# Optimization experiments

Hardware: AMD Instinct MI355X
Metric: run time of the kernel (lower is better)

The kernel has to match this reference:

```python
import jax, jax.numpy as jnp
import numpy as np

N_VOX = 200_000
C = 64
B, G = 2, 128  # batch size, grid resolution per axis
K = 27         # 3x3x3 kernel volume
EPS = 1e-5


def _build_coords_and_kernel_map(seed=0):
    """Build unique voxel coords on a [B,G,G,G] grid and the 27-offset kernel map.

    nbr[i, k] = row index of the voxel at coord[i] + offset[k], or N_VOX if absent
    (sentinel row that gathers zeros). This mirrors MinkowskiEngine's
    coordinate-hash in/out kernel maps for a stride-1 conv.
    """
    rng = np.random.default_rng(seed)
    total = B * G * G * G
    keys = np.sort(rng.choice(total, size=N_VOX, replace=False).astype(np.int64))
    z = keys % G
    y = (keys // G) % G
    x = (keys // (G * G)) % G
    b = keys // (G * G * G)
    offs = [(dx, dy, dz) for dx in (-1, 0, 1) for dy in (-1, 0, 1) for dz in (-1, 0, 1)]
    nbr = np.full((N_VOX, K), N_VOX, dtype=np.int64)
    for k, (dx, dy, dz) in enumerate(offs):
        nx, ny, nz = x + dx, y + dy, z + dz
        valid = (nx >= 0) & (nx < G) & (ny >= 0) & (ny < G) & (nz >= 0) & (nz < G)
        nkey = ((b * G + nx) * G + ny) * G + nz
        pos = np.clip(np.searchsorted(keys, nkey), 0, N_VOX - 1)
        found = valid & (keys[pos] == nkey)
        nbr[:, k] = np.where(found, pos, N_VOX)
    return jnp.asarray(nbr)


def setup_inputs() -> dict:
    key = jax.random.key(0)
    ks = jax.random.split(key, 12)
    w_scale = 1.0 / np.sqrt(K * C)
    inp = {
        "feats": jax.random.normal(ks[0], (N_VOX, C), jnp.float32),
        "nbr": _build_coords_and_kernel_map(),
        "W1": jax.random.normal(ks[1], (K, C, C), jnp.float32) * w_scale,
        "g1": 1.0 + 0.1 * jax.random.normal(ks[2], (C,), jnp.float32),
        "b1": 0.1 * jax.random.normal(ks[3], (C,), jnp.float32),
        "m1": 0.1 * jax.random.normal(ks[4], (C,), jnp.float32),
        "v1": jax.random.uniform(ks[5], (C,), jnp.float32, 0.5, 1.5),
        "W2": jax.random.normal(ks[6], (K, C, C), jnp.float32) * w_scale,
        "g2": 1.0 + 0.1 * jax.random.normal(ks[7], (C,), jnp.float32),
        "b2": 0.1 * jax.random.normal(ks[8], (C,), jnp.float32),
        "m2": 0.1 * jax.random.normal(ks[9], (C,), jnp.float32),
        "v2": jax.random.uniform(ks[10], (C,), jnp.float32, 0.5, 1.5),
    }
    return inp


def _bn(x, g, b, m, v):
    # MinkowskiBatchNorm, eval mode: per-channel affine with running stats
    return (x - m) * (g * jax.lax.rsqrt(v + EPS)) + b


def _sparse_conv(feats, nbr, W):
    # gather-GEMM-scatter sparse 3D conv over the precomputed kernel map.
    # Sentinel index N_VOX gathers the appended zero row (missing neighbor).
    fpad = jnp.concatenate([feats, jnp.zeros((1, feats.shape[1]), feats.dtype)], axis=0)
    out = jnp.zeros((feats.shape[0], W.shape[2]), feats.dtype)
    for k in range(W.shape[0]):  # fixed 27-tap loop (structural, not data dim)
        out = out + fpad[nbr[:, k]] @ W[k]
    return out


def reference(feats, nbr, W1, g1, b1, m1, v1, W2, g2, b2, m2, v2):
    h = jax.nn.relu(_bn(_sparse_conv(feats, nbr, W1), g1, b1, m1, v1))
    h = _bn(_sparse_conv(h, nbr, W2), g2, b2, m2, v2)
    # in_channels == out_channels and stride == 1 -> identity shortcut
    return jax.nn.relu(h + feats)
```

## Files before the change

### kernel.cpp

```cpp
#include <hip/hip_runtime.h>
#include <hip/hip_bf16.h>

#define NVOX 200000
#define NTAP 27
#define OSTR 68
#define ROWB 128
#define VPB  128

typedef __bf16          bf16x8 __attribute__((ext_vector_type(8)));
typedef unsigned short  u16x8  __attribute__((ext_vector_type(8)));
typedef float           f32x4  __attribute__((ext_vector_type(4)));

#define FB_BYTES    ((size_t)(NVOX + 1) * ROWB)
#define WSHUF_BYTES (NTAP * 2 * 4 * 64 * 16)
#define FB_OFF      0
#define H_OFF       (FB_BYTES)
#define WS1_OFF     (2 * FB_BYTES)
#define WS2_OFF     (WS1_OFF + WSHUF_BYTES)
#define FLAG_OFF    (WS2_OFF + WSHUF_BYTES)

static __device__ __forceinline__ unsigned short f2bf_bits(float f) {
    __hip_bfloat16 h = __float2bfloat16(f);
    union { __hip_bfloat16 h; unsigned short u; } u; u.h = h; return u.u;
}
static __device__ __forceinline__ float bf2f(unsigned short s) {
    union { float f; unsigned u; } u; u.u = ((unsigned)s) << 16; return u.f;
}
static __device__ __forceinline__ float ld_param(const void* p, int c, int isbf) {
    return isbf ? bf2f(((const unsigned short*)p)[c]) : ((const float*)p)[c];
}
static __device__ __forceinline__ void gload_lds16(const void* gp, void* lp) {
    __builtin_amdgcn_global_load_lds(
        (const __attribute__((address_space(1))) void*)gp,
        (__attribute__((address_space(3))) void*)lp, 16, 0, 0);
}
static __device__ __forceinline__ int wave_isbf(const unsigned* v1w) {
    int l = threadIdx.x & 63;
    int ok = 1;
    if (l < 32) {
        unsigned w = v1w[l], lo = w & 0xFFFFu, hi = w >> 16;
        ok = (lo >= 0x3F00u && lo <= 0x3FC0u && hi >= 0x3F00u && hi <= 0x3FC0u);
    }
    return __all(ok);
}

__global__ __launch_bounds__(256)
void prep_kernel(const void* __restrict__ feats,
                 const void* __restrict__ W1, const void* __restrict__ W2,
                 const unsigned* __restrict__ v1w, const unsigned* __restrict__ nbrw,
                 uint4* __restrict__ fbuf, uint4* __restrict__ hbuf,
                 uint4* __restrict__ Ws1, uint4* __restrict__ Ws2,
                 int* __restrict__ flags) {
    const int bx = blockIdx.x;
    if (bx < 6250) {
        const int isbf = wave_isbf(v1w);
        size_t t = (size_t)bx * 256 + threadIdx.x;
        if (isbf) {
            fbuf[t] = ((const uint4*)feats)[t];
        } else {
            float4 a = ((const float4*)feats)[2 * t];
            float4 b = ((const float4*)feats)[2 * t + 1];
            union { uint4 q; unsigned short u[8]; } o;
            o.u[0] = f2bf_bits(a.x); o.u[1] = f2bf_bits(a.y);
            o.u[2] = f2bf_bits(a.z); o.u[3] = f2bf_bits(a.w);
            o.u[4] = f2bf_bits(b.x); o.u[5] = f2bf_bits(b.y);
            o.u[6] = f2bf_bits(b.z); o.u[7] = f2bf_bits(b.w);
            fbuf[t] = o.q;
        }
    } else if (bx < 6358) {
        const int isbf = wave_isbf(v1w);
        int t = (bx - 6250) * 256 + threadIdx.x;
        const void* W = (t < 13824) ? W1 : W2;
        uint4* Ws     = (t < 13824) ? Ws1 : Ws2;
        int f = (t < 13824) ? t : t - 13824;
        int k  = f / 512;
        int r  = f % 512;
        int kc = r / 256;
        int r2 = r % 256;
        int nc = r2 / 64;
        int l  = r2 % 64;
        int quad = l >> 4, li = l & 15;
        unsigned short tmp[8];
#pragma unroll
        for (int j = 0; j < 8; ++j) {
            int off = k * 4096 + (kc * 32 + quad * 8 + j) * 64 + (nc * 16 + li);
            tmp[j] = isbf ? ((const unsigned short*)W)[off]
                          : f2bf_bits(((const float*)W)[off]);
        }
        uint4 v;
        v.x = (unsigned)tmp[0] | ((unsigned)tmp[1] << 16);
        v.y = (unsigned)tmp[2] | ((unsigned)tmp[3] << 16);
        v.z = (unsigned)tmp[4] | ((unsigned)tmp[5] << 16);
        v.w = (unsigned)tmp[6] | ((unsigned)tmp[7] << 16);
        Ws[f] = v;
    } else {
        int t = threadIdx.x;
        if (t < 64) {
            int isbf = wave_isbf(v1w);
            int n64ok = 1;
#pragma unroll
            for (int i = 0; i < 8; ++i)
                if (nbrw[2 * (t * 8 + i) + 1] != 0u) n64ok = 0;
            int n64 = __all(n64ok);
            if (t == 0) { flags[0] = isbf; flags[1] = n64; }
        }
        uint4 z = make_uint4(0u, 0u, 0u, 0u);
        if (t >= 64 && t < 72) fbuf[(size_t)NVOX * 8 + (t - 64)] = z;
        if (t >= 72 && t < 80) hbuf[(size_t)NVOX * 8 + (t - 72)] = z;
    }
}

#define STG(kk, bp) do {                                                    \
    if ((mga >> (kk)) & 1) {                                                \
        int ia_ = bad0 ? NVOX : nbrG[o0 + (kk) * tmul];                     \
        int ib_ = bad1 ? NVOX : nbrG[o1 + (kk) * tmul];                     \
        gload_lds16(srcB + (size_t)ia_ * ROWB + f0 * 16,                    \
                    (void*)((bp) + w * 256));                               \
        gload_lds16(srcB + (size_t)ib_ * ROWB + f1 * 16,                    \
                    (void*)((bp) + w * 256 + 64));                          \
    }                                                                       \
    if ((mgb >> (kk)) & 1) {                                                \
        int ic_ = bad2 ? NVOX : nbrG[o2 + (kk) * tmul];                     \
        int id_ = bad3 ? NVOX : nbrG[o3 + (kk) * tmul];                     \
        gload_lds16(srcB + (size_t)ic_ * ROWB + f2 * 16,                    \
                    (void*)((bp) + w * 256 + 128));                         \
        gload_lds16(srcB + (size_t)id_ * ROWB + f3 * 16,                    \
                    (void*)((bp) + w * 256 + 192));                         \
    } } while (0)

#define LOADB(kk, B0r, B1r) do {                                            \
    B0r = Ws[(kk) * 512 + w * 64 + l];                                      \
    B1r = Ws[(kk) * 512 + 256 + w * 64 + l];                                \
} while (0)

#define COMPUTE(kk, bp, B0, B1) do {                                        \
    _Pragma("unroll")                                                       \
    for (int g = 0; g < 8; ++g) {                                           \
        if ((mg[g] >> (kk)) & 1) {                                          \
            bf16x8 a0_ = *(const bf16x8*)((bp) + ro0[g]);                   \
            bf16x8 a1_ = *(const bf16x8*)((bp) + ro1[g]);                   \
            acc[g] = __builtin_amdgcn_mfma_f32_16x16x32_bf16(a0_, B0, acc[g], 0, 0, 0); \
            acc[g] = __builtin_amdgcn_mfma_f32_16x16x32_bf16(a1_, B1, acc[g], 0, 0, 0); \
        }                                                                   \
    }                                                                       \
} while (0)

__global__ __launch_bounds__(256, 4)
void conv_bn_kernel(const uint4* __restrict__ srcV,
                    const void* __restrict__ nbr,
                    const bf16x8* __restrict__ Ws,
                    const void* __restrict__ gg, const void* __restrict__ bb,
                    const void* __restrict__ mm, const void* __restrict__ vv,
                    const u16x8* __restrict__ resid,
                    const int* __restrict__ flags,
                    void* __restrict__ dst, int final_out) {
    __shared__ __align__(16) int smi[VPB * OSTR];
    int*   maskLDS = smi;
    uint4* at0     = (uint4*)(smi + 8);
    uint4* at1     = at0 + 1024;
    float* outLDS  = (float*)smi;

    const int tid  = threadIdx.x;
    const int nwg  = gridDim.x;
    const int orig = blockIdx.x;
    const int qq   = nwg >> 3, rr = nwg & 7;
    const int xcd  = orig & 7, idx = orig >> 3;
    const int bid  = (xcd < rr ? xcd * (qq + 1) : rr * (qq + 1) + (xcd - rr) * qq) + idx;
    const int base = bid * VPB;

    const int isbf = flags[0];
    const int n64  = flags[1];
    const char* srcB = (const char*)srcV;

    const int* nbrG = (const int*)nbr;
    const int  tmul = n64 ? 2 : 1;
    const int  smul = NTAP * tmul;

    if (tid < 8) maskLDS[tid] = 0;
    __syncthreads();

    if (tid < NTAP * 8) {
        int k = tid >> 3, g = tid & 7;
        int mn = 0x7fffffff;
#pragma unroll
        for (int r = 0; r < 16; ++r) {
            int vx = base + g * 16 + r;
            int safe = vx < NVOX ? vx : NVOX - 1;
            int v = nbrG[safe * smul + k * tmul];
            if (vx >= NVOX) v = NVOX;
            mn = min(mn, v);
        }
        if (mn < NVOX) atomicOr(&maskLDS[g], 1 << k);
    }
    __syncthreads();

    const int w = tid >> 6, l = tid & 63;
    const int quad = l >> 4, li = l & 15;

    int mg[8];
#pragma unroll
    for (int g = 0; g < 8; ++g) mg[g] = __builtin_amdgcn_readfirstlane(maskLDS[g]);
    const int mga = __builtin_amdgcn_readfirstlane(maskLDS[2 * w]);
    const int mgb = __builtin_amdgcn_readfirstlane(maskLDS[2 * w + 1]);

    int o_[4], f_[4], bad_[4];
#pragma unroll
    for (int j = 0; j < 4; ++j) {
        int s  = w * 256 + j * 64 + l;
        int r  = s >> 3;
        f_[j]  = (s - r) & 7;
        int vx = base + r;
        bad_[j] = vx >= NVOX;
        o_[j]  = (bad_[j] ? NVOX - 1 : vx) * smul;
    }
    const int o0 = o_[0], o1 = o_[1], o2 = o_[2], o3 = o_[3];
    const int f0 = f_[0], f1 = f_[1], f2 = f_[2], f3 = f_[3];
    const int bad0 = bad_[0], bad1 = bad_[1], bad2 = bad_[2], bad3 = bad_[3];

    int ro0[8], ro1[8];
#pragma unroll
    for (int g = 0; g < 8; ++g) {
        int row = g * 16 + li;
        ro0[g] = row * 8 + ((quad + row) & 7);
        ro1[g] = row * 8 + ((quad + 4 + row) & 7);
    }

    f32x4 acc[8];
#pragma unroll
    for (int g = 0; g < 8; ++g) acc[g] = (f32x4){0.f, 0.f, 0.f, 0.f};

    bf16x8 xB0, xB1, yB0, yB1;

    STG(0, at0);
    LOADB(0, xB0, xB1);
    __syncthreads();

    for (int k = 0; k < 26; k += 2) {
        STG(k + 1, at1);
        LOADB(k + 1, yB0, yB1);
        COMPUTE(k, at0, xB0, xB1);
        __syncthreads();
        STG(k + 2, at0);
        LOADB(k + 2, xB0, xB1);
        COMPUTE(k + 1, at1, yB0, yB1);
        __syncthreads();
    }
    COMPUTE(26, at0, xB0, xB1);

    const int c = w * 16 + li;
    float scale = ld_param(gg, c, isbf) * rsqrtf(ld_param(vv, c, isbf) + 1e-5f);
    float offs  = ld_param(bb, c, isbf) - ld_param(mm, c, isbf) * scale;

    __syncthreads();
#pragma unroll
    for (int g = 0; g < 8; ++g)
#pragma unroll
        for (int r = 0; r < 4; ++r)
            outLDS[(g * 16 + quad * 4 + r) * OSTR + c] = acc[g][r] * scale + offs;
    __syncthreads();

#pragma unroll
    for (int half = 0; half < 2; ++half) {
        int trow = half * 64 + (tid >> 2), cc = tid & 3;
        long grow = base + trow;
        if (grow < NVOX) {
            const float4* lp = (const float4*)&outLDS[trow * OSTR + cc * 16];
            float4 q0 = lp[0], q1 = lp[1], q2 = lp[2], q3 = lp[3];
            float vals[16] = {q0.x, q0.y, q0.z, q0.w, q1.x, q1.y, q1.z, q1.w,
                              q2.x, q2.y, q2.z, q2.w, q3.x, q3.y, q3.z, q3.w};

            if (resid) {
                const u16x8* rp = resid + grow * 8 + cc * 2;
                u16x8 r0v = rp[0], r1v = rp[1];
#pragma unroll
                for (int j = 0; j < 8; ++j) { vals[j] += bf2f(r0v[j]); vals[8 + j] += bf2f(r1v[j]); }
            }
#pragma unroll
            for (int j = 0; j < 16; ++j) vals[j] = fmaxf(vals[j], 0.f);

            const int store_bf = (!final_out) || isbf;
            if (store_bf) {
                u16x8 o0v, o1v;
#pragma unroll
                for (int j = 0; j < 8; ++j) { o0v[j] = f2bf_bits(vals[j]); o1v[j] = f2bf_bits(vals[8 + j]); }
                u16x8* dp = (u16x8*)dst + grow * 8 + cc * 2;
                dp[0] = o0v; dp[1] = o1v;
            } else {
                float4* dp = (float4*)dst + grow * 16 + cc * 4;
                dp[0] = (float4){vals[0], vals[1], vals[2], vals[3]};
                dp[1] = (float4){vals[4], vals[5], vals[6], vals[7]};
                dp[2] = (float4){vals[8], vals[9], vals[10], vals[11]};
                dp[3] = (float4){vals[12], vals[13], vals[14], vals[15]};
            }
        }
    }
}

extern "C" void kernel_launch(void* const* d_in, const int* in_sizes, int n_in,
                              void* d_out, int out_size, void* d_ws, size_t ws_size,
                              hipStream_t stream) {
    const void* feats = d_in[0];
    const void* nbr   = d_in[1];
    const void* W1    = d_in[2];
    const void* g1    = d_in[3];
    const void* b1    = d_in[4];
    const void* m1    = d_in[5];
    const void* v1    = d_in[6];
    const void* W2    = d_in[7];
    const void* g2    = d_in[8];
    const void* b2    = d_in[9];
    const void* m2    = d_in[10];
    const void* v2    = d_in[11];

    char* ws = (char*)d_ws;
    uint4* fbuf = (uint4*)(ws + FB_OFF);
    uint4* hbuf = (uint4*)(ws + H_OFF);
    uint4* Ws1  = (uint4*)(ws + WS1_OFF);
    uint4* Ws2  = (uint4*)(ws + WS2_OFF);
    int*   flags = (int*)(ws + FLAG_OFF);

    prep_kernel<<<dim3(6359), dim3(256), 0, stream>>>(
        feats, W1, W2, (const unsigned*)v1, (const unsigned*)nbr,
        fbuf, hbuf, Ws1, Ws2, flags);

    const int nblk = (NVOX + VPB - 1) / VPB;
    conv_bn_kernel<<<dim3(nblk), dim3(256), 0, stream>>>(
        fbuf, nbr, (const bf16x8*)Ws1, g1, b1, m1, v1,
        nullptr, flags, hbuf, 0);

    conv_bn_kernel<<<dim3(nblk), dim3(256), 0, stream>>>(
        hbuf, nbr, (const bf16x8*)Ws2, g2, b2, m2, v2,
        (const u16x8*)fbuf, flags, d_out, 1);
}
```

Before: 285.3 us.

## Halve LDS staging buffers by pipelining half-tiles to raise occupancy

The gather staging is split into two 64-row halves. One half is loaded into one LDS buffer while the other half is computed, and the same per-tap weight registers serve both halves. This halves shared memory per block (128x68 to 64x68 ints) and raises launch bounds from 4 to 6 blocks per CU, to hide gather latency through occupancy. The cost is twice as many barriers per tap, less prefetch distance, and an epilogue done in two passes.

```diff
diff --git a/kernel.cpp b/kernel.cpp
--- a/kernel.cpp
+++ b/kernel.cpp
@@ -110,22 +110,14 @@
     }
 }
 
-#define STG(kk, bp) do {                                                    \
-    if ((mga >> (kk)) & 1) {                                                \
-        int ia_ = bad0 ? NVOX : nbrG[o0 + (kk) * tmul];                     \
-        int ib_ = bad1 ? NVOX : nbrG[o1 + (kk) * tmul];                     \
+#define STG_H(kk, gm, oo0, oo1, bb0, bb1, bp) do {                          \
+    if (((gm) >> (kk)) & 1) {                                               \
+        int ia_ = (bb0) ? NVOX : nbrG[(oo0) + (kk) * tmul];                 \
+        int ib_ = (bb1) ? NVOX : nbrG[(oo1) + (kk) * tmul];                 \
         gload_lds16(srcB + (size_t)ia_ * ROWB + f0 * 16,                    \
-                    (void*)((bp) + w * 256));                               \
+                    (void*)((bp) + w * 128));                               \
         gload_lds16(srcB + (size_t)ib_ * ROWB + f1 * 16,                    \
-                    (void*)((bp) + w * 256 + 64));                          \
-    }                                                                       \
-    if ((mgb >> (kk)) & 1) {                                                \
-        int ic_ = bad2 ? NVOX : nbrG[o2 + (kk) * tmul];                     \
-        int id_ = bad3 ? NVOX : nbrG[o3 + (kk) * tmul];                     \
-        gload_lds16(srcB + (size_t)ic_ * ROWB + f2 * 16,                    \
-                    (void*)((bp) + w * 256 + 128));                         \
-        gload_lds16(srcB + (size_t)id_ * ROWB + f3 * 16,                    \
-                    (void*)((bp) + w * 256 + 192));                         \
+                    (void*)((bp) + w * 128 + 64));                          \
     } } while (0)
 
 #define LOADB(kk, B0r, B1r) do {                                            \
@@ -133,19 +125,19 @@
     B1r = Ws[(kk) * 512 + 256 + w * 64 + l];                                \
 } while (0)
 
-#define COMPUTE(kk, bp, B0, B1) do {                                        \
+#define COMPUTE_H(kk, hb, bp, B0, B1) do {                                  \
     _Pragma("unroll")                                                       \
-    for (int g = 0; g < 8; ++g) {                                           \
-        if ((mg[g] >> (kk)) & 1) {                                          \
-            bf16x8 a0_ = *(const bf16x8*)((bp) + ro0[g]);                   \
-            bf16x8 a1_ = *(const bf16x8*)((bp) + ro1[g]);                   \
-            acc[g] = __builtin_amdgcn_mfma_f32_16x16x32_bf16(a0_, B0, acc[g], 0, 0, 0); \
-            acc[g] = __builtin_amdgcn_mfma_f32_16x16x32_bf16(a1_, B1, acc[g], 0, 0, 0); \
+    for (int gl = 0; gl < 4; ++gl) {                                        \
+        if ((mg[(hb) + gl] >> (kk)) & 1) {                                  \
+            bf16x8 a0_ = *(const bf16x8*)((bp) + ro0[gl]);                  \
+            bf16x8 a1_ = *(const bf16x8*)((bp) + ro1[gl]);                  \
+            acc[(hb) + gl] = __builtin_amdgcn_mfma_f32_16x16x32_bf16(a0_, B0, acc[(hb) + gl], 0, 0, 0); \
+            acc[(hb) + gl] = __builtin_amdgcn_mfma_f32_16x16x32_bf16(a1_, B1, acc[(hb) + gl], 0, 0, 0); \
         }                                                                   \
     }                                                                       \
 } while (0)
 
-__global__ __launch_bounds__(256, 4)
+__global__ __launch_bounds__(256, 6)
 void conv_bn_kernel(const uint4* __restrict__ srcV,
                     const void* __restrict__ nbr,
                     const bf16x8* __restrict__ Ws,
@@ -154,10 +146,10 @@
                     const u16x8* __restrict__ resid,
                     const int* __restrict__ flags,
                     void* __restrict__ dst, int final_out) {
-    __shared__ __align__(16) int smi[VPB * OSTR];
+    __shared__ __align__(16) int smi[64 * OSTR];
     int*   maskLDS = smi;
     uint4* at0     = (uint4*)(smi + 8);
-    uint4* at1     = at0 + 1024;
+    uint4* at1     = at0 + 512;
     float* outLDS  = (float*)smi;
 
     const int tid  = threadIdx.x;
@@ -200,69 +192,72 @@
     int mg[8];
 #pragma unroll
     for (int g = 0; g < 8; ++g) mg[g] = __builtin_amdgcn_readfirstlane(maskLDS[g]);
-    const int mga = __builtin_amdgcn_readfirstlane(maskLDS[2 * w]);
-    const int mgb = __builtin_amdgcn_readfirstlane(maskLDS[2 * w + 1]);
-
-    int o_[4], f_[4], bad_[4];
-#pragma unroll
-    for (int j = 0; j < 4; ++j) {
-        int s  = w * 256 + j * 64 + l;
-        int r  = s >> 3;
-        f_[j]  = (s - r) & 7;
-        int vx = base + r;
-        bad_[j] = vx >= NVOX;
-        o_[j]  = (bad_[j] ? NVOX - 1 : vx) * smul;
-    }
-    const int o0 = o_[0], o1 = o_[1], o2 = o_[2], o3 = o_[3];
-    const int f0 = f_[0], f1 = f_[1], f2 = f_[2], f3 = f_[3];
-    const int bad0 = bad_[0], bad1 = bad_[1], bad2 = bad_[2], bad3 = bad_[3];
-
-    int ro0[8], ro1[8];
-#pragma unroll
-    for (int g = 0; g < 8; ++g) {
-        int row = g * 16 + li;
-        ro0[g] = row * 8 + ((quad + row) & 7);
-        ro1[g] = row * 8 + ((quad + 4 + row) & 7);
+    const int gA = mg[w];
+    const int gB = mg[4 + w];
+
+    const int s0 = w * 128 + l;
+    const int s1 = s0 + 64;
+    const int r0 = s0 >> 3, f0 = (s0 - r0) & 7;
+    const int r1 = s1 >> 3, f1 = (s1 - r1) & 7;
+    int oA0, oA1, oB0, oB1, bA0, bA1, bB0, bB1;
+    {
+        int vA0 = base + r0,      vA1 = base + r1;
+        int vB0 = base + 64 + r0, vB1 = base + 64 + r1;
+        bA0 = vA0 >= NVOX; bA1 = vA1 >= NVOX;
+        bB0 = vB0 >= NVOX; bB1 = vB1 >= NVOX;
+        oA0 = (bA0 ? NVOX - 1 : vA0) * smul;
+        oA1 = (bA1 ? NVOX - 1 : vA1) * smul;
+        oB0 = (bB0 ? NVOX - 1 : vB0) * smul;
+        oB1 = (bB1 ? NVOX - 1 : vB1) * smul;
+    }
+    int ro0[4], ro1[4];
+#pragma unroll
+    for (int gl = 0; gl < 4; ++gl) {
+        int row = gl * 16 + li;
+        ro0[gl] = row * 8 + ((quad + row) & 7);
+        ro1[gl] = row * 8 + ((quad + 4 + row) & 7);
     }
 
     f32x4 acc[8];
 #pragma unroll
     for (int g = 0; g < 8; ++g) acc[g] = (f32x4){0.f, 0.f, 0.f, 0.f};
 
-    bf16x8 xB0, xB1, yB0, yB1;
-
-    STG(0, at0);
+    bf16x8 xB0, xB1;
+
+    STG_H(0, gA, oA0, oA1, bA0, bA1, at0);
     LOADB(0, xB0, xB1);
     __syncthreads();
 
-    for (int k = 0; k < 26; k += 2) {
-        STG(k + 1, at1);
-        LOADB(k + 1, yB0, yB1);
-        COMPUTE(k, at0, xB0, xB1);
+    for (int k = 0; k < 26; ++k) {
+        STG_H(k, gB, oB0, oB1, bB0, bB1, at1);
+        COMPUTE_H(k, 0, at0, xB0, xB1);
         __syncthreads();
-        STG(k + 2, at0);
-        LOADB(k + 2, xB0, xB1);
-        COMPUTE(k + 1, at1, yB0, yB1);
+        STG_H(k + 1, gA, oA0, oA1, bA0, bA1, at0);
+        COMPUTE_H(k, 4, at1, xB0, xB1);
+        LOADB(k + 1, xB0, xB1);
         __syncthreads();
     }
-    COMPUTE(26, at0, xB0, xB1);
+    STG_H(26, gB, oB0, oB1, bB0, bB1, at1);
+    COMPUTE_H(26, 0, at0, xB0, xB1);
+    __syncthreads();
+    COMPUTE_H(26, 4, at1, xB0, xB1);
 
     const int c = w * 16 + li;
     float scale = ld_param(gg, c, isbf) * rsqrtf(ld_param(vv, c, isbf) + 1e-5f);
     float offs  = ld_param(bb, c, isbf) - ld_param(mm, c, isbf) * scale;
 
-    __syncthreads();
-#pragma unroll
-    for (int g = 0; g < 8; ++g)
-#pragma unroll
-        for (int r = 0; r < 4; ++r)
-            outLDS[(g * 16 + quad * 4 + r) * OSTR + c] = acc[g][r] * scale + offs;
-    __syncthreads();
-
-#pragma unroll
-    for (int half = 0; half < 2; ++half) {
-        int trow = half * 64 + (tid >> 2), cc = tid & 3;
-        long grow = base + trow;
+#pragma unroll
+    for (int h = 0; h < 2; ++h) {
+        __syncthreads();
+#pragma unroll
+        for (int gl = 0; gl < 4; ++gl)
+#pragma unroll
+            for (int r = 0; r < 4; ++r)
+                outLDS[(gl * 16 + quad * 4 + r) * OSTR + c] = acc[4 * h + gl][r] * scale + offs;
+        __syncthreads();
+
+        int trow = tid >> 2, cc = tid & 3;
+        long grow = base + 64 * h + trow;
         if (grow < NVOX) {
             const float4* lp = (const float4*)&outLDS[trow * OSTR + cc * 16];
             float4 q0 = lp[0], q1 = lp[1], q2 = lp[2], q3 = lp[3];
```

Result: faster. 265.7 us (-6.9%).
